# Performance work log

Hardware: AMD Instinct MI355X
Metric: run time of the kernel (lower is better)

Reference implementation:

```python
import math
import jax, jax.numpy as jnp
import numpy as np

# TreeAttention (HiP-style hierarchical top-k mask) hyperparameters
K = 64          # self.k: retained keys per query
W0 = 64         # self.w: initial coarse window
SCALE_UP = 2.0
OVERSAMPLE = 1.5
NEG = -32000.0  # masked score fill used inside the pruning loop
FMIN = -1e30    # masked score fill for final softmax


def _gather_rows(m, idx):
    # m: [N, C, H], idx: [N, A, Z] -> [N, A, Z, H]
    return jnp.take_along_axis(m[:, None, :, :], idx[:, :, :, None], axis=2)


def _masked_scores(q, k, xs, xs_mask, value):
    # jax equivalent of masked_bmm_masked_indices (sampled_addmm on a CSR mask):
    # only compute q . k[xs] at the Z listed columns per query row.
    C = k.shape[1]
    kg = _gather_rows(k, jnp.minimum(xs, C - 1))          # [N, A, Z, H]
    s = jnp.einsum('nah,nazh->naz', q, kg)
    return jnp.where(xs_mask > 0.5, s, value)


def _dedup_rows(ps):
    # ps: [R, L] sorted ascending per row. Replicates torch
    # unique_consecutive(return_inverse) + per-row min-subtract + scatter:
    # compact distinct values to the front, fill the rest with -1.
    first = jnp.ones((ps.shape[0], 1), dtype=bool)
    is_new = jnp.concatenate([first, ps[:, 1:] != ps[:, :-1]], axis=1)
    ranks = jnp.cumsum(is_new, axis=1) - 1                # rank of distinct value in row
    rows = jnp.arange(ps.shape[0])[:, None]
    out = jnp.full_like(ps, -1)
    return out.at[rows, ranks].set(ps)  # duplicate ranks write identical values


def _forward_mask(q, k):
    N, T_SRC, HID = k.shape
    _, T_DST, _ = q.shape
    start = T_SRC - T_DST + 1
    tsrcs = jnp.arange(start, start + T_DST, dtype=jnp.float32)[None, :, None]  # [1,T_DST,1]
    w = W0
    ws = jnp.full((N, T_DST, 1), float(W0), dtype=jnp.float32)
    max_pixels = max(int(round(K * OVERSAMPLE)), W0)
    pixels = jnp.broadcast_to(jnp.arange(max_pixels, dtype=jnp.int32)[None, None, :],
                              (N, T_DST, max_pixels))
    pmask = jnp.broadcast_to((jnp.arange(max_pixels) < W0).astype(jnp.float32)[None, None, :],
                             (N, T_DST, max_pixels))
    MAX_SU = int(math.ceil(SCALE_UP))
    while True:  # static loop: w doubles 64 -> 4096, 7 iterations
        is_last = (w == T_SRC)
        Z = pixels.shape[-1]
        # --- topk_mask: score the current candidate pixels, keep top tks ---
        txs = jnp.round(pixels * (tsrcs / ws)).astype(jnp.int32)
        scores = _masked_scores(q, k, txs, pmask, NEG)
        mult = 1.0 if is_last else OVERSAMPLE
        tks = jnp.clip(jnp.round(ws / tsrcs * K * mult), 1.0,
                       jnp.minimum(ws - 1.0, float(Z - 1))).astype(jnp.int32)  # [N,T_DST,1]
        tks_max = int(math.ceil(min(w - 1, Z - 1, K * mult)))
        _, idx = jax.lax.top_k(scores, tks_max)
        new_pixels = jnp.take_along_axis(pixels, idx, axis=-1)
        new_pmask = (jnp.arange(tks_max)[None, None, :] < tks).astype(jnp.float32)
        pixels = jnp.pad(new_pixels, ((0, 0), (0, 0), (0, Z - tks_max)))
        pmask = jnp.pad(new_pmask, ((0, 0), (0, 0), (0, Z - tks_max)))
        # --- update per-row window, then resize pixels into the finer grid ---
        ws_new = jnp.minimum(tsrcs, ws * SCALE_UP)
        scale = ws_new / ws
        ps_start = jnp.round(pixels * scale).astype(jnp.int32)
        ps_end = jnp.round((pixels + 1) * scale).astype(jnp.int32)
        ps = jnp.broadcast_to(ps_start[..., None], (N, T_DST, Z, MAX_SU))
        counts = (ps_end - ps_start)[..., None]
        reps = jnp.arange(MAX_SU, dtype=jnp.float32)[None, None, None, :] * pmask[..., None]
        ps = ps + jnp.minimum(reps, jnp.maximum(counts - 1, 0).astype(jnp.float32)).astype(jnp.int32)
        ps = jnp.sort(ps.reshape(N * T_DST, Z * MAX_SU), axis=-1)
        ps = _dedup_rows(ps).reshape(N, T_DST, -1)
        pmask = (ps >= 0).astype(jnp.float32)
        pixels = jnp.where(ps < 0, 0, ps)
        max_z = K if is_last else int(round(K * 2))
        pixels = pixels[..., :max_z]
        pmask = pmask[..., :max_z]
        ws = ws_new
        if is_last:
            break
        w = min(T_SRC, w * SCALE_UP)
    return pixels, pmask  # CSR mask: per-query column indices + validity mask


def setup_inputs() -> dict:
    key = jax.random.key(0)
    kq, kk, kv = jax.random.split(key, 3)
    N, T_DST, T_SRC, HID = 8, 512, 4096, 64
    q = jax.random.normal(kq, (N, T_DST, HID), dtype=jnp.float32)
    k = jax.random.normal(kk, (N, T_SRC, HID), dtype=jnp.float32)
    v = jax.random.normal(kv, (N, T_SRC, HID), dtype=jnp.float32)
    return {"q": q, "k": k, "v": v}


def reference(q, k, v):
    pixels, pmask = _forward_mask(q, k)          # [N,T_DST,K] int, [N,T_DST,K] {0,1}
    kg = _gather_rows(k, pixels)                 # [N,T_DST,K,H]
    vg = _gather_rows(v, pixels)
    s = jnp.einsum('nah,nazh->naz', q, kg)
    s = jnp.where(pmask > 0.5, s, FMIN)
    p = jax.nn.softmax(s, axis=-1)
    return jnp.einsum('naz,nazh->nah', p, vg)    # [N, T_DST, HID]
```

## Files before the change

kernel.cpp:

```cpp
#include <hip/hip_runtime.h>
#include <math.h>


#define TSRC_N 4096
#define HID_N  64
#define NEGV   -32000.0f

__global__ __launch_bounds__(64)
void tree_attn_kernel(const float* __restrict__ q,
                      const float* __restrict__ k,
                      const float* __restrict__ v,
                      float* __restrict__ out)
{
    const int row  = blockIdx.x;
    const int n    = row >> 9;
    const float tsrc = (float)(3585 + (row & 511));
    const int lane = threadIdx.x;

    __shared__ __align__(16) unsigned int key_s[128];
    __shared__ __align__(16) unsigned int bm[128];
    __shared__ int                        pix_s[128];
    __shared__ unsigned char              msk_s[128];
    __shared__ __align__(8) unsigned int  pp_s[128];

    const float* qrow = q + (size_t)row * HID_N;
    const float* kb   = k + (size_t)n * TSRC_N * HID_N;
    const float* vb   = v + (size_t)n * TSRC_N * HID_N;

    auto dot_f32 = [&](int tx) -> float {
        const float4* k4 = (const float4*)(kb + (size_t)tx * HID_N);
        float a0 = 0.f, a1 = 0.f, a2 = 0.f, a3 = 0.f;
        #pragma unroll
        for (int h4 = 0; h4 < HID_N / 4; ++h4) {
            const float4 kv = k4[h4];
            a0 = fmaf(kv.x, qrow[h4 * 4 + 0], a0);
            a1 = fmaf(kv.y, qrow[h4 * 4 + 1], a1);
            a2 = fmaf(kv.z, qrow[h4 * 4 + 2], a2);
            a3 = fmaf(kv.w, qrow[h4 * 4 + 3], a3);
        }
        return (a0 + a1) + (a2 + a3);
    };
    auto flip32 = [](float s) -> unsigned int {
        const unsigned int u = __float_as_uint(s);
        return u ^ ((unsigned)((int)u >> 31) | 0x80000000u);
    };

    pix_s[lane]      = lane;
    pix_s[lane + 64] = lane + 64;
    msk_s[lane]      = 1;
    msk_s[lane + 64] = 0;
    __syncthreads();

    float ws = 64.0f;
    int Z = 96;

    for (int it = 0; it < 7; ++it) {
        const bool  last    = (it == 6);
        const float mult    = last ? 1.0f : 1.5f;
        const int   tks_max = (it == 0) ? 63 : (last ? 64 : 96);
        const int   max_z   = last ? 64 : 128;
        const int   e1      = lane + 64;

        const float r = tsrc / ws;
        unsigned int key0 = 0, key1 = 0;
        {
            float s0 = NEGV;
            if (msk_s[lane]) {
                int tx = (int)rintf((float)pix_s[lane] * r);
                tx = tx < (TSRC_N - 1) ? tx : (TSRC_N - 1);
                s0 = dot_f32(tx);
            }
            key0 = flip32(s0);
        }
        if (e1 < Z) {
            float s1 = NEGV;
            if (msk_s[e1]) {
                int tx = (int)rintf((float)pix_s[e1] * r);
                tx = tx < (TSRC_N - 1) ? tx : (TSRC_N - 1);
                s1 = dot_f32(tx);
            }
            key1 = flip32(s1);
        }
        key_s[lane] = key0;
        key_s[e1]   = key1;
        bm[lane]    = 0u;
        bm[e1]      = 0u;
        __syncthreads();

        int r0 = 0, r1 = 0;
        #pragma unroll 8
        for (int j = 0; j < 128; j += 4) {
            const uint4 kk = *(const uint4*)&key_s[j];
            r0 += (int)(kk.x > key0) + (int)(kk.y > key0)
                + (int)(kk.z > key0) + (int)(kk.w > key0);
            r1 += (int)(kk.x > key1) + (int)(kk.y > key1)
                + (int)(kk.z > key1) + (int)(kk.w > key1);
        }

        float x = ws / tsrc;
        x *= 64.0f;
        x *= mult;
        float t = rintf(x);
        t = fmaxf(1.0f, fminf(t, fminf(ws - 1.0f, (float)(Z - 1))));
        const int tks = (int)t;

        const float ws_new = fminf(tsrc, ws * 2.0f);
        const float scale  = ws_new / ws;

        if (lane == 0) atomicOr(&bm[0], 1u);
        if (r0 < tks_max) {
            const int p  = pix_s[lane];
            int s0 = (int)rintf((float)p * scale);
            s0 = s0 < (TSRC_N - 1) ? s0 : (TSRC_N - 1);
            atomicOr(&bm[s0 >> 5], 1u << (s0 & 31));
            if (r0 < tks) {
                const int s1i = (int)rintf((float)(p + 1) * scale);
                if (s1i - s0 >= 2) {
                    const int c = s0 + 1;
                    atomicOr(&bm[c >> 5], 1u << (c & 31));
                }
            }
        }
        if (e1 < Z && r1 < tks_max) {
            const int p  = pix_s[e1];
            int s0 = (int)rintf((float)p * scale);
            s0 = s0 < (TSRC_N - 1) ? s0 : (TSRC_N - 1);
            atomicOr(&bm[s0 >> 5], 1u << (s0 & 31));
            if (r1 < tks) {
                const int s1i = (int)rintf((float)(p + 1) * scale);
                if (s1i - s0 >= 2) {
                    const int c = s0 + 1;
                    atomicOr(&bm[c >> 5], 1u << (c & 31));
                }
            }
        }
        __syncthreads();

        const uint2 w2 = *(const uint2*)&bm[2 * lane];
        const int c = __popc(w2.x) + __popc(w2.y);
        int scan = c;
        #pragma unroll
        for (int off = 1; off < 64; off <<= 1) {
            const int o = __shfl_up(scan, off);
            if (lane >= off) scan += o;
        }
        int pref = scan - c;
        pix_s[lane] = 0;  pix_s[e1] = 0;
        msk_s[lane] = 0;  msk_s[e1] = 0;
        __syncthreads();

        unsigned int wv = w2.x;
        int base = lane << 6;
        while (wv) {
            if (pref >= max_z) break;
            const int b = __ffs(wv) - 1;
            wv &= wv - 1u;
            pix_s[pref] = base + b;
            msk_s[pref] = 1;
            ++pref;
        }
        wv = w2.y;
        base += 32;
        while (wv) {
            if (pref >= max_z) break;
            const int b = __ffs(wv) - 1;
            wv &= wv - 1u;
            pix_s[pref] = base + b;
            msk_s[pref] = 1;
            ++pref;
        }
        __syncthreads();

        ws = ws_new;
        Z  = max_z;
    }

    {
        const int pix = pix_s[lane];
        float sfin = -1e30f;
        if (msk_s[lane]) sfin = dot_f32(pix);
        float m = sfin;
        #pragma unroll
        for (int off = 32; off > 0; off >>= 1)
            m = fmaxf(m, __shfl_xor(m, off));
        const float e = __expf(sfin - m);
        float ssum = e;
        #pragma unroll
        for (int off = 32; off > 0; off >>= 1)
            ssum += __shfl_xor(ssum, off);
        const float p = e / ssum;
        pp_s[2 * lane]     = __float_as_uint(p);
        pp_s[2 * lane + 1] = (unsigned int)pix;
    }
    __syncthreads();

    {
        float acc = 0.f;
        #pragma unroll 4
        for (int j = 0; j < 64; ++j) {
            const uint2 pp = *(const uint2*)&pp_s[2 * j];
            acc = fmaf(__uint_as_float(pp.x),
                       vb[(size_t)pp.y * HID_N + lane], acc);
        }
        out[(size_t)row * HID_N + lane] = acc;
    }
}

extern "C" void kernel_launch(void* const* d_in, const int* in_sizes, int n_in,
                              void* d_out, int out_size, void* d_ws, size_t ws_size,
                              hipStream_t stream) {
    const float* q = (const float*)d_in[0];
    const float* k = (const float*)d_in[1];
    const float* v = (const float*)d_in[2];
    float* out = (float*)d_out;
    const int rows = in_sizes[0] / HID_N;
    tree_attn_kernel<<<rows, 64, 0, stream>>>(q, k, v, out);
}
```

Measured before the change: 166.6 us.

## Pack four independent query rows per block and use wave barriers

Each block now runs four wavefronts, each handling its own query row with a private slice of shared memory, so the grid shrinks fourfold. Block-wide __syncthreads are replaced by wave-level barriers because a row's data is only touched by its own wave. The aim is to cut per-block launch and barrier overhead and raise how many waves each CU can hold. Correctness relies on wave-level LDS ordering being enough, and the launch assumes the row count divides by four.

Result: no change. 163.9 us (-1.7%).

```diff
diff --git a/kernel.cpp b/kernel.cpp
--- a/kernel.cpp
+++ b/kernel.cpp
@@ -6,22 +6,28 @@
 #define HID_N  64
 #define NEGV   -32000.0f
 
-__global__ __launch_bounds__(64)
+__global__ __launch_bounds__(256)
 void tree_attn_kernel(const float* __restrict__ q,
                       const float* __restrict__ k,
                       const float* __restrict__ v,
                       float* __restrict__ out)
 {
-    const int row  = blockIdx.x;
+    const int wid  = __builtin_amdgcn_readfirstlane((int)(threadIdx.x >> 6));
+    const int lane = threadIdx.x & 63;
+    const int row  = (blockIdx.x << 2) + wid;
     const int n    = row >> 9;
     const float tsrc = (float)(3585 + (row & 511));
-    const int lane = threadIdx.x;
-
-    __shared__ __align__(16) unsigned int key_s[128];
-    __shared__ __align__(16) unsigned int bm[128];
-    __shared__ int                        pix_s[128];
-    __shared__ unsigned char              msk_s[128];
-    __shared__ __align__(8) unsigned int  pp_s[128];
+
+    __shared__ __align__(16) unsigned int key_s[4][128];
+    __shared__ __align__(16) unsigned int bm[4][128];
+    __shared__ int                        pix_s[4][128];
+    __shared__ unsigned char              msk_s[4][128];
+    __shared__ __align__(8) unsigned int  pp_s[4][128];
+    unsigned int* const keyw = key_s[wid];
+    unsigned int* const bmw  = bm[wid];
+    int* const           pixw = pix_s[wid];
+    unsigned char* const mskw = msk_s[wid];
+    unsigned int* const  ppw  = pp_s[wid];
 
     const float* qrow = q + (size_t)row * HID_N;
     const float* kb   = k + (size_t)n * TSRC_N * HID_N;
@@ -45,11 +51,11 @@
         return u ^ ((unsigned)((int)u >> 31) | 0x80000000u);
     };
 
-    pix_s[lane]      = lane;
-    pix_s[lane + 64] = lane + 64;
-    msk_s[lane]      = 1;
-    msk_s[lane + 64] = 0;
-    __syncthreads();
+    pixw[lane]      = lane;
+    pixw[lane + 64] = lane + 64;
+    mskw[lane]      = 1;
+    mskw[lane + 64] = 0;
+    __builtin_amdgcn_wave_barrier();
 
     float ws = 64.0f;
     int Z = 96;
@@ -65,8 +71,8 @@
         unsigned int key0 = 0, key1 = 0;
         {
             float s0 = NEGV;
-            if (msk_s[lane]) {
-                int tx = (int)rintf((float)pix_s[lane] * r);
+            if (mskw[lane]) {
+                int tx = (int)rintf((float)pixw[lane] * r);
                 tx = tx < (TSRC_N - 1) ? tx : (TSRC_N - 1);
                 s0 = dot_f32(tx);
             }
@@ -74,23 +80,23 @@
         }
         if (e1 < Z) {
             float s1 = NEGV;
-            if (msk_s[e1]) {
-                int tx = (int)rintf((float)pix_s[e1] * r);
+            if (mskw[e1]) {
+                int tx = (int)rintf((float)pixw[e1] * r);
                 tx = tx < (TSRC_N - 1) ? tx : (TSRC_N - 1);
                 s1 = dot_f32(tx);
             }
             key1 = flip32(s1);
         }
-        key_s[lane] = key0;
-        key_s[e1]   = key1;
-        bm[lane]    = 0u;
-        bm[e1]      = 0u;
-        __syncthreads();
+        keyw[lane] = key0;
+        keyw[e1]   = key1;
+        bmw[lane]  = 0u;
+        bmw[e1]    = 0u;
+        __builtin_amdgcn_wave_barrier();
 
         int r0 = 0, r1 = 0;
         #pragma unroll 8
         for (int j = 0; j < 128; j += 4) {
-            const uint4 kk = *(const uint4*)&key_s[j];
+            const uint4 kk = *(const uint4*)&keyw[j];
             r0 += (int)(kk.x > key0) + (int)(kk.y > key0)
                 + (int)(kk.z > key0) + (int)(kk.w > key0);
             r1 += (int)(kk.x > key1) + (int)(kk.y > key1)
@@ -107,36 +113,36 @@
         const float ws_new = fminf(tsrc, ws * 2.0f);
         const float scale  = ws_new / ws;
 
-        if (lane == 0) atomicOr(&bm[0], 1u);
+        if (lane == 0) atomicOr(&bmw[0], 1u);
         if (r0 < tks_max) {
-            const int p  = pix_s[lane];
+            const int p  = pixw[lane];
             int s0 = (int)rintf((float)p * scale);
             s0 = s0 < (TSRC_N - 1) ? s0 : (TSRC_N - 1);
-            atomicOr(&bm[s0 >> 5], 1u << (s0 & 31));
+            atomicOr(&bmw[s0 >> 5], 1u << (s0 & 31));
             if (r0 < tks) {
                 const int s1i = (int)rintf((float)(p + 1) * scale);
                 if (s1i - s0 >= 2) {
                     const int c = s0 + 1;
-                    atomicOr(&bm[c >> 5], 1u << (c & 31));
+                    atomicOr(&bmw[c >> 5], 1u << (c & 31));
                 }
             }
         }
         if (e1 < Z && r1 < tks_max) {
-            const int p  = pix_s[e1];
+            const int p  = pixw[e1];
             int s0 = (int)rintf((float)p * scale);
             s0 = s0 < (TSRC_N - 1) ? s0 : (TSRC_N - 1);
-            atomicOr(&bm[s0 >> 5], 1u << (s0 & 31));
+            atomicOr(&bmw[s0 >> 5], 1u << (s0 & 31));
             if (r1 < tks) {
                 const int s1i = (int)rintf((float)(p + 1) * scale);
                 if (s1i - s0 >= 2) {
                     const int c = s0 + 1;
-                    atomicOr(&bm[c >> 5], 1u << (c & 31));
+                    atomicOr(&bmw[c >> 5], 1u << (c & 31));
                 }
             }
         }
-        __syncthreads();
-
-        const uint2 w2 = *(const uint2*)&bm[2 * lane];
+        __builtin_amdgcn_wave_barrier();
+
+        const uint2 w2 = *(const uint2*)&bmw[2 * lane];
         const int c = __popc(w2.x) + __popc(w2.y);
         int scan = c;
         #pragma unroll
@@ -145,9 +151,9 @@
             if (lane >= off) scan += o;
         }
         int pref = scan - c;
-        pix_s[lane] = 0;  pix_s[e1] = 0;
-        msk_s[lane] = 0;  msk_s[e1] = 0;
-        __syncthreads();
+        pixw[lane] = 0;  pixw[e1] = 0;
+        mskw[lane] = 0;  mskw[e1] = 0;
+        __builtin_amdgcn_wave_barrier();
 
         unsigned int wv = w2.x;
         int base = lane << 6;
@@ -155,8 +161,8 @@
             if (pref >= max_z) break;
             const int b = __ffs(wv) - 1;
             wv &= wv - 1u;
-            pix_s[pref] = base + b;
-            msk_s[pref] = 1;
+            pixw[pref] = base + b;
+            mskw[pref] = 1;
             ++pref;
         }
         wv = w2.y;
@@ -165,20 +171,20 @@
             if (pref >= max_z) break;
             const int b = __ffs(wv) - 1;
             wv &= wv - 1u;
-            pix_s[pref] = base + b;
-            msk_s[pref] = 1;
+            pixw[pref] = base + b;
+            mskw[pref] = 1;
             ++pref;
         }
-        __syncthreads();
+        __builtin_amdgcn_wave_barrier();
 
         ws = ws_new;
         Z  = max_z;
     }
 
     {
-        const int pix = pix_s[lane];
+        const int pix = pixw[lane];
         float sfin = -1e30f;
-        if (msk_s[lane]) sfin = dot_f32(pix);
+        if (mskw[lane]) sfin = dot_f32(pix);
         float m = sfin;
         #pragma unroll
         for (int off = 32; off > 0; off >>= 1)
@@ -189,16 +195,16 @@
         for (int off = 32; off > 0; off >>= 1)
             ssum += __shfl_xor(ssum, off);
         const float p = e / ssum;
-        pp_s[2 * lane]     = __float_as_uint(p);
-        pp_s[2 * lane + 1] = (unsigned int)pix;
+        ppw[2 * lane]     = __float_as_uint(p);
+        ppw[2 * lane + 1] = (unsigned int)pix;
     }
-    __syncthreads();
+    __builtin_amdgcn_wave_barrier();
 
     {
         float acc = 0.f;
         #pragma unroll 4
         for (int j = 0; j < 64; ++j) {
-            const uint2 pp = *(const uint2*)&pp_s[2 * j];
+            const uint2 pp = *(const uint2*)&ppw[2 * j];
             acc = fmaf(__uint_as_float(pp.x),
                        vb[(size_t)pp.y * HID_N + lane], acc);
         }
@@ -214,5 +220,5 @@
     const float* v = (const float*)d_in[2];
     float* out = (float*)d_out;
     const int rows = in_sizes[0] / HID_N;
-    tree_attn_kernel<<<rows, 64, 0, stream>>>(q, k, v, out);
+    tree_attn_kernel<<<(rows + 3) / 4, 256, 0, stream>>>(q, k, v, out);
 }
```
